# Kernel optimization log

Hardware: AMD Instinct MI355X
Metric: run time of the kernel (lower is better)

Reference implementation:

```python
import jax, jax.numpy as jnp
import numpy as np

EMBED_DIM = 1024
NUM_HEADS = 16
NUM_GROUPS = 4
HEAD_DIM = EMBED_DIM // NUM_HEADS
REPEAT = NUM_HEADS // NUM_GROUPS
MAX_TIME = 128
MAX_FREQ = 8


def build_relative_index(q_len, k_len, freq_size=MAX_FREQ, max_time=MAX_TIME, max_freq=MAX_FREQ):
    # static (numpy) construction; shapes are compile-time constants under jit
    q_time = q_len // max_freq
    k_time = k_len // max_freq
    qt = np.arange(q_time) + (k_time - q_time)
    q_coords = np.stack(np.meshgrid(qt, np.arange(freq_size), indexing='ij')).reshape(2, -1)
    k_coords = np.stack(np.meshgrid(np.arange(k_time), np.arange(freq_size), indexing='ij')).reshape(2, -1)
    rel = q_coords[:, :, None] - k_coords[:, None, :]  # [2, Nq, Nk]
    rel_t = np.clip(rel[0], -max_time + 1, max_time - 1) + max_time - 1
    rel_f = np.clip(rel[1], -max_freq + 1, max_freq - 1) + max_freq - 1
    return jnp.asarray(rel_t, jnp.int32), jnp.asarray(rel_f, jnp.int32)


def setup_inputs() -> dict:
    key = jax.random.key(0)
    ks = jax.random.split(key, 11)
    B, N, D, Nc = 2, 512, EMBED_DIM, 1536
    s = 0.02
    return {
        'q': jax.random.normal(ks[0], (B, N, D), jnp.float32),
        'k': jax.random.normal(ks[1], (B, N, D), jnp.float32),
        'v': jax.random.normal(ks[2], (B, N, D), jnp.float32),
        'attn_cache_k': jax.random.normal(ks[3], (B * NUM_HEADS, HEAD_DIM, Nc), jnp.float32),
        'attn_cache_v': jax.random.normal(ks[4], (B * NUM_HEADS, Nc, HEAD_DIM), jnp.float32),
        'Wq': jax.random.normal(ks[5], (D, D), jnp.float32) * s,
        'Wk': jax.random.normal(ks[6], (D, HEAD_DIM * NUM_GROUPS), jnp.float32) * s,
        'Wv': jax.random.normal(ks[7], (D, HEAD_DIM * NUM_GROUPS), jnp.float32) * s,
        'Wo': jax.random.normal(ks[8], (D, D), jnp.float32) * s,
        'emb_t': jax.random.normal(ks[9], (2 * MAX_TIME - 1, HEAD_DIM), jnp.float32) * s,
        'emb_f': jax.random.normal(ks[10], (2 * MAX_FREQ - 1, HEAD_DIM), jnp.float32) * s,
    }


def reference(q, k, v, attn_cache_k, attn_cache_v, Wq, Wk, Wv, Wo, emb_t, emb_f):
    B, N, D = q.shape
    H, G, hd, r = NUM_HEADS, NUM_GROUPS, HEAD_DIM, REPEAT
    # projections (no bias); head layout matches torch view: [B, N, H, hd] -> [B*H, N, hd]
    qp = (q @ Wq).reshape(B, N, H, hd).transpose(0, 2, 1, 3).reshape(B * H, N, hd)
    kp = (k @ Wk).reshape(B, N, G, hd).transpose(0, 2, 3, 1).reshape(B * G, hd, N)  # transposed K
    vp = (v @ Wv).reshape(B, N, G, hd).transpose(0, 2, 1, 3).reshape(B * G, N, hd)
    # GQA: repeat_interleave kv heads to query heads
    kp = jnp.repeat(kp, r, axis=0)
    vp = jnp.repeat(vp, r, axis=0)
    # streaming cache concat + slide
    k_full = jnp.concatenate([attn_cache_k, kp], axis=-1)            # [B*H, hd, Nk]
    new_cache_k = k_full[:, :, -attn_cache_k.shape[-1]:]
    v_full = jnp.concatenate([attn_cache_v, vp], axis=1)             # [B*H, Nk, hd]
    new_cache_v = v_full[:, -attn_cache_v.shape[1]:, :]
    Nk = k_full.shape[-1]
    qs = qp * (hd ** -0.5)
    scores = jnp.einsum('bid,bdj->bij', qs, k_full)                  # [B*H, N, Nk]
    rel_t, rel_f = build_relative_index(N, Nk)
    rel_emb = emb_t[rel_t] + emb_f[rel_f]                            # [N, Nk, hd]
    bias = jnp.einsum('bid,ijd->bij', qs, rel_emb)
    attn = jax.nn.softmax(scores + bias, axis=-1)
    ao = jnp.einsum('bij,bjd->bid', attn, v_full)                    # [B*H, N, hd]
    ao = ao.reshape(B, H, N, hd).transpose(2, 0, 1, 3).reshape(N, B, D)
    out = (ao @ Wo).transpose(1, 0, 2)                               # [B, N, D]
    return out, new_cache_k, new_cache_v
```

## Files before the change

### kernel.cpp

```cpp
#include <hip/hip_runtime.h>
#include <math.h>

typedef _Float16 half_t;
typedef _Float16 half8  __attribute__((ext_vector_type(8)));
typedef _Float16 half4v __attribute__((ext_vector_type(4)));
typedef float    floatx4 __attribute__((ext_vector_type(4)));

#define LOG2E 1.44269504088896f

static __device__ __forceinline__ floatx4 mfma16(half8 a, half8 b, floatx4 c) {
    return __builtin_amdgcn_mfma_f32_16x16x32_f16(a, b, c, 0, 0, 0);
}
static __device__ __forceinline__ floatx4 mfma16x16(half4v a, half4v b, floatx4 c) {
    return __builtin_amdgcn_mfma_f32_16x16x16f16(a, b, c, 0, 0, 0);
}

__global__ __launch_bounds__(256) void prep(const float* __restrict__ cache_k,
                                            const float* __restrict__ cache_v,
                                            const float* __restrict__ Wq,
                                            const float* __restrict__ Wk,
                                            const float* __restrict__ Wv,
                                            const float* __restrict__ Wo,
                                            const float* __restrict__ emb_t,
                                            const float* __restrict__ emb_f,
                                            half_t* __restrict__ Kc,
                                            half_t* __restrict__ Vc4,
                                            float* __restrict__ out_k,
                                            float* __restrict__ out_v,
                                            half_t* __restrict__ WqT,
                                            half_t* __restrict__ WkvT,
                                            half_t* __restrict__ WoT,
                                            half_t* __restrict__ embc)
{
    const int tid = threadIdx.x;
    const int z = blockIdx.z;
    __shared__ float t[64][65];
    if (z == 0) {
        const int bh = blockIdx.y, j0 = blockIdx.x * 64;
        const bool shift = (j0 >= 512);
        #pragma unroll
        for (int i2 = 0; i2 < 4; i2++) {
            int idx = i2 * 256 + tid;
            int d = idx >> 4, j4 = (idx & 15) * 4;
            float4 vv = *(const float4*)&cache_k[((size_t)bh * 64 + d) * 1536 + j0 + j4];
            *(float4*)&t[d][j4] = vv;
            if (shift) *(float4*)&out_k[((size_t)bh * 64 + d) * 1536 + j0 - 512 + j4] = vv;
        }
        __syncthreads();
        #pragma unroll
        for (int i2 = 0; i2 < 2; i2++) {
            int idx = i2 * 256 + tid;
            int j = idx >> 3, db = (idx & 7) * 8;
            half8 o;
            #pragma unroll
            for (int u = 0; u < 8; u++) o[u] = (half_t)t[db + u][j];
            *(half8*)&Kc[((size_t)bh * 1536 + j0 + j) * 64 + db] = o;
        }
    } else if (z == 1) {
        const int bh = blockIdx.y, j0 = blockIdx.x * 64;
        const bool shift = (j0 >= 512);
        #pragma unroll
        for (int i2 = 0; i2 < 4; i2++) {
            int idx = i2 * 256 + tid;
            int j = idx >> 4, d4 = (idx & 15) * 4;
            float4 vv = *(const float4*)&cache_v[((size_t)bh * 1536 + j0 + j) * 64 + d4];
            *(float4*)&t[j][d4] = vv;
            if (shift) *(float4*)&out_v[((size_t)bh * 1536 + j0 + j - 512) * 64 + d4] = vv;
        }
        __syncthreads();
        #pragma unroll
        for (int i2 = 0; i2 < 4; i2++) {
            int idx = i2 * 256 + tid;
            int jc = idx >> 6, d = idx & 63;
            half4v o;
            #pragma unroll
            for (int u = 0; u < 4; u++) o[u] = (half_t)t[jc * 4 + u][d];
            *(half4v*)&Vc4[(((size_t)bh * 384 + (j0 >> 2) + jc) * 64 + d) * 4] = o;
        }
    } else {
        const int id = blockIdx.y * 24 + blockIdx.x;
        const float* src; half_t* dst; int Ncols, n0, k0;
        if (id < 256)      { src = Wq; dst = WqT; Ncols = 1024; n0 = (id & 15) * 64; k0 = (id >> 4) * 64; }
        else if (id < 320) { int q2 = id - 256; src = Wk; dst = WkvT; Ncols = 256; n0 = (q2 & 3) * 64; k0 = (q2 >> 2) * 64; }
        else if (id < 384) { int q2 = id - 320; src = Wv; dst = WkvT + 256 * 1024; Ncols = 256; n0 = (q2 & 3) * 64; k0 = (q2 >> 2) * 64; }
        else if (id < 640) { int q2 = id - 384; src = Wo; dst = WoT; Ncols = 1024; n0 = (q2 & 15) * 64; k0 = (q2 >> 4) * 64; }
        else if (id < 720) {
            int idx = (id - 640) * 256 + tid;
            int row = idx >> 6, col = idx & 63;
            float val = 0.f;
            if (row < 255) val = emb_t[row * 64 + col];
            else if (row >= 256 && row < 271) val = emb_f[(row - 256) * 64 + col];
            embc[idx] = (half_t)val;
            return;
        } else return;
        #pragma unroll
        for (int i2 = 0; i2 < 4; i2++) {
            int idx = i2 * 256 + tid;
            int r = idx >> 4, c4 = (idx & 15) * 4;
            *(float4*)&t[r][c4] = *(const float4*)&src[(size_t)(k0 + r) * Ncols + n0 + c4];
        }
        __syncthreads();
        #pragma unroll
        for (int i2 = 0; i2 < 2; i2++) {
            int idx = i2 * 256 + tid;
            int n = idx >> 3, kb = (idx & 7) * 8;
            half8 o;
            #pragma unroll
            for (int u = 0; u < 8; u++) o[u] = (half_t)t[kb + u][n];
            *(half8*)&dst[(size_t)(n0 + n) * 1024 + k0 + kb] = o;
        }
    }
}

__global__ __launch_bounds__(512) void proj(int phase,
                                            const float* __restrict__ qin,
                                            const float* __restrict__ kin,
                                            const float* __restrict__ vin,
                                            const half_t* __restrict__ AO,
                                            const half_t* __restrict__ WqT,
                                            const half_t* __restrict__ WkvT,
                                            const half_t* __restrict__ WoT,
                                            half_t* __restrict__ qs_h,
                                            half_t* __restrict__ kp_h,
                                            half_t* __restrict__ Vp4,
                                            float* __restrict__ out,
                                            float* __restrict__ out_k,
                                            float* __restrict__ out_v)
{
    __shared__ __align__(16) half_t As[2][2][64 * 72];
    __shared__ __align__(16) half_t Bs[2][2][64 * 72];
    const int id = blockIdx.x;
    int task, m0, n0;
    const float* Af = nullptr; const half_t* Ah = nullptr; const half_t* Bt;
    if (phase == 1)      { task = 2; m0 = (id >> 4) * 64; n0 = (id & 15) * 64; Ah = AO; Bt = WoT; }
    else if (id < 256)   { task = 0; m0 = (id >> 4) * 64; n0 = (id & 15) * 64; Af = qin; Bt = WqT; }
    else { task = 1; int t = id - 256; m0 = (t >> 3) * 64; n0 = (t & 7) * 64;
           Af = (n0 < 256) ? kin : vin; Bt = WkvT; }

    const int tid = threadIdx.x;
    const int kh = tid >> 8, t8 = tid & 255;
    const int w4 = (tid >> 6) & 3, l = tid & 63;
    const int quad = l >> 4, lr = l & 15, wm = w4 >> 1, wn = w4 & 1;
    const int arow = t8 >> 2, acol = (t8 & 3) * 16;
    const int kbase = kh * 512;

    {
        int kk = kbase;
        if (Af) {
            float4 f0 = *(const float4*)&Af[(size_t)(m0 + arow) * 1024 + kk + acol];
            float4 f1 = *(const float4*)&Af[(size_t)(m0 + arow) * 1024 + kk + acol + 4];
            float4 f2 = *(const float4*)&Af[(size_t)(m0 + arow) * 1024 + kk + acol + 8];
            float4 f3 = *(const float4*)&Af[(size_t)(m0 + arow) * 1024 + kk + acol + 12];
            half8 h0, h1;
            h0[0]=(half_t)f0.x; h0[1]=(half_t)f0.y; h0[2]=(half_t)f0.z; h0[3]=(half_t)f0.w;
            h0[4]=(half_t)f1.x; h0[5]=(half_t)f1.y; h0[6]=(half_t)f1.z; h0[7]=(half_t)f1.w;
            h1[0]=(half_t)f2.x; h1[1]=(half_t)f2.y; h1[2]=(half_t)f2.z; h1[3]=(half_t)f2.w;
            h1[4]=(half_t)f3.x; h1[5]=(half_t)f3.y; h1[6]=(half_t)f3.z; h1[7]=(half_t)f3.w;
            *(half8*)&As[kh][0][arow * 72 + acol] = h0;
            *(half8*)&As[kh][0][arow * 72 + acol + 8] = h1;
        } else {
            *(half8*)&As[kh][0][arow * 72 + acol]     = *(const half8*)&Ah[(size_t)(m0 + arow) * 1024 + kk + acol];
            *(half8*)&As[kh][0][arow * 72 + acol + 8] = *(const half8*)&Ah[(size_t)(m0 + arow) * 1024 + kk + acol + 8];
        }
        *(half8*)&Bs[kh][0][arow * 72 + acol]     = *(const half8*)&Bt[(size_t)(n0 + arow) * 1024 + kk + acol];
        *(half8*)&Bs[kh][0][arow * 72 + acol + 8] = *(const half8*)&Bt[(size_t)(n0 + arow) * 1024 + kk + acol + 8];
    }
    __syncthreads();

    floatx4 zero = {0.f, 0.f, 0.f, 0.f};
    floatx4 acc[2][2];
    acc[0][0] = zero; acc[0][1] = zero; acc[1][0] = zero; acc[1][1] = zero;

    float4 pf0, pf1, pf2, pf3; half8 ph0, ph1, pb0, pb1;
    for (int it = 0; it < 8; ++it) {
        if (it < 7) {
            int kk = kbase + (it + 1) * 64;
            if (Af) {
                pf0 = *(const float4*)&Af[(size_t)(m0 + arow) * 1024 + kk + acol];
                pf1 = *(const float4*)&Af[(size_t)(m0 + arow) * 1024 + kk + acol + 4];
                pf2 = *(const float4*)&Af[(size_t)(m0 + arow) * 1024 + kk + acol + 8];
                pf3 = *(const float4*)&Af[(size_t)(m0 + arow) * 1024 + kk + acol + 12];
            } else {
                ph0 = *(const half8*)&Ah[(size_t)(m0 + arow) * 1024 + kk + acol];
                ph1 = *(const half8*)&Ah[(size_t)(m0 + arow) * 1024 + kk + acol + 8];
            }
            pb0 = *(const half8*)&Bt[(size_t)(n0 + arow) * 1024 + kk + acol];
            pb1 = *(const half8*)&Bt[(size_t)(n0 + arow) * 1024 + kk + acol + 8];
        }
        const half_t* Ab = &As[kh][it & 1][0];
        const half_t* Bb = &Bs[kh][it & 1][0];
        #pragma unroll
        for (int ks = 0; ks < 2; ++ks) {
            half8 a0 = *(const half8*)&Ab[(wm * 32 + lr) * 72 + ks * 32 + quad * 8];
            half8 a1 = *(const half8*)&Ab[(wm * 32 + 16 + lr) * 72 + ks * 32 + quad * 8];
            half8 b0 = *(const half8*)&Bb[(wn * 32 + lr) * 72 + ks * 32 + quad * 8];
            half8 b1 = *(const half8*)&Bb[(wn * 32 + 16 + lr) * 72 + ks * 32 + quad * 8];
            acc[0][0] = mfma16(a0, b0, acc[0][0]);
            acc[0][1] = mfma16(a0, b1, acc[0][1]);
            acc[1][0] = mfma16(a1, b0, acc[1][0]);
            acc[1][1] = mfma16(a1, b1, acc[1][1]);
        }
        __syncthreads();
        if (it < 7) {
            int buf = (it + 1) & 1;
            if (Af) {
                half8 h0, h1;
                h0[0]=(half_t)pf0.x; h0[1]=(half_t)pf0.y; h0[2]=(half_t)pf0.z; h0[3]=(half_t)pf0.w;
                h0[4]=(half_t)pf1.x; h0[5]=(half_t)pf1.y; h0[6]=(half_t)pf1.z; h0[7]=(half_t)pf1.w;
                h1[0]=(half_t)pf2.x; h1[1]=(half_t)pf2.y; h1[2]=(half_t)pf2.z; h1[3]=(half_t)pf2.w;
                h1[4]=(half_t)pf3.x; h1[5]=(half_t)pf3.y; h1[6]=(half_t)pf3.z; h1[7]=(half_t)pf3.w;
                *(half8*)&As[kh][buf][arow * 72 + acol] = h0;
                *(half8*)&As[kh][buf][arow * 72 + acol + 8] = h1;
            } else {
                *(half8*)&As[kh][buf][arow * 72 + acol] = ph0;
                *(half8*)&As[kh][buf][arow * 72 + acol + 8] = ph1;
            }
            *(half8*)&Bs[kh][buf][arow * 72 + acol] = pb0;
            *(half8*)&Bs[kh][buf][arow * 72 + acol + 8] = pb1;
            __syncthreads();
        }
    }

    float* M = (float*)&Bs[0][0][0];
    if (kh == 1) {
        #pragma unroll
        for (int mi = 0; mi < 2; mi++)
            #pragma unroll
            for (int ni = 0; ni < 2; ni++)
                #pragma unroll
                for (int r = 0; r < 4; r++)
                    M[(wm * 32 + mi * 16 + quad * 4 + r) * 66 + wn * 32 + ni * 16 + lr] = acc[mi][ni][r];
    }
    __syncthreads();
    if (kh == 0) {
        #pragma unroll
        for (int mi = 0; mi < 2; mi++)
            #pragma unroll
            for (int ni = 0; ni < 2; ni++)
                #pragma unroll
                for (int r = 0; r < 4; r++)
                    acc[mi][ni][r] += M[(wm * 32 + mi * 16 + quad * 4 + r) * 66 + wn * 32 + ni * 16 + lr];
    }

    if (task == 0) {
        if (kh == 0) {
            #pragma unroll
            for (int mi = 0; mi < 2; mi++)
                #pragma unroll
                for (int ni = 0; ni < 2; ni++)
                    #pragma unroll
                    for (int r = 0; r < 4; r++) {
                        int m = m0 + wm * 32 + mi * 16 + quad * 4 + r;
                        int n = n0 + wn * 32 + ni * 16 + lr;
                        qs_h[(size_t)m * 1024 + n] = (half_t)(acc[mi][ni][r] * (0.125f * LOG2E));
                    }
        }
    } else if (task == 2) {
        if (kh == 0) {
            #pragma unroll
            for (int mi = 0; mi < 2; mi++)
                #pragma unroll
                for (int ni = 0; ni < 2; ni++)
                    #pragma unroll
                    for (int r = 0; r < 4; r++) {
                        int m = m0 + wm * 32 + mi * 16 + quad * 4 + r;
                        int n = n0 + wn * 32 + ni * 16 + lr;
                        out[(size_t)m * 1024 + n] = acc[mi][ni][r];
                    }
        }
    } else {
        float* Ct = (float*)&As[0][0][0];
        if (kh == 0) {
            #pragma unroll
            for (int mi = 0; mi < 2; mi++)
                #pragma unroll
                for (int ni = 0; ni < 2; ni++)
                    #pragma unroll
                    for (int r = 0; r < 4; r++)
                        Ct[(wn * 32 + ni * 16 + lr) * 68 + wm * 32 + mi * 16 + quad * 4 + r] = acc[mi][ni][r];
        }
        __syncthreads();
        if (kh == 0) {
            const int b = m0 >> 9, jm0 = m0 & 511;
            if (n0 < 256) {
                int gg = n0 >> 6;
                {
                    int d = t8 >> 2, jc = (t8 & 3) * 16;
                    float4 vv[4];
                    #pragma unroll
                    for (int u = 0; u < 4; u++) vv[u] = *(float4*)&Ct[d * 68 + jc + u * 4];
                    #pragma unroll
                    for (int t = 0; t < 4; t++)
                        #pragma unroll
                        for (int u = 0; u < 4; u++)
                            *(float4*)&out_k[((size_t)((b * 16 + gg * 4 + t) * 64 + d)) * 1536 + 1024 + jm0 + jc + u * 4] = vv[u];
                }
                {
                    int j = t8 >> 2, dc = (t8 & 3) * 16;
                    half8 o0, o1;
                    #pragma unroll
                    for (int u = 0; u < 8; u++) o0[u] = (half_t)Ct[(dc + u) * 68 + j];
                    #pragma unroll
                    for (int u = 0; u < 8; u++) o1[u] = (half_t)Ct[(dc + 8 + u) * 68 + j];
                    *(half8*)&kp_h[((size_t)(b * 512 + jm0 + j)) * 256 + n0 + dc] = o0;
                    *(half8*)&kp_h[((size_t)(b * 512 + jm0 + j)) * 256 + n0 + dc + 8] = o1;
                }
            } else {
                int gg = (n0 - 256) >> 6;
                {
                    int j = t8 >> 2, dc = (t8 & 3) * 16;
                    float4 vv[4];
                    #pragma unroll
                    for (int u = 0; u < 4; u++) {
                        float4 x;
                        x.x = Ct[(dc + u * 4 + 0) * 68 + j];
                        x.y = Ct[(dc + u * 4 + 1) * 68 + j];
                        x.z = Ct[(dc + u * 4 + 2) * 68 + j];
                        x.w = Ct[(dc + u * 4 + 3) * 68 + j];
                        vv[u] = x;
                    }
                    #pragma unroll
                    for (int t = 0; t < 4; t++)
                        #pragma unroll
                        for (int u = 0; u < 4; u++)
                            *(float4*)&out_v[(((size_t)(b * 16 + gg * 4 + t) * 1536) + 1024 + jm0 + j) * 64 + dc + u * 4] = vv[u];
                }
                {
                    int d = t8 >> 2, jc16 = (t8 & 3) * 16;
                    #pragma unroll
                    for (int u = 0; u < 4; u++) {
                        half4v o;
                        #pragma unroll
                        for (int s2 = 0; s2 < 4; s2++) o[s2] = (half_t)Ct[d * 68 + jc16 + u * 4 + s2];
                        *(half4v*)&Vp4[(((size_t)(b * 4 + gg) * 128 + ((jm0 + jc16) >> 2) + u) * 64 + d) * 4] = o;
                    }
                }
            }
        }
    }
}

__global__ __launch_bounds__(512, 4) void flash(const half_t* __restrict__ qs_h,
                                                const half_t* __restrict__ Kc,
                                                const half_t* __restrict__ kp_h,
                                                const half_t* __restrict__ Vc4,
                                                const half_t* __restrict__ Vp4,
                                                const half_t* __restrict__ embc,
                                                half_t* __restrict__ AO)
{
    __shared__ __align__(16) unsigned char smem_raw[61824];
    half_t* bt = (half_t*)smem_raw;

    const int bh = blockIdx.x, b = bh >> 4, h = bh & 15, g = h >> 2;
    const int i0 = blockIdx.y * 32;
    const int tid = threadIdx.x, jh = tid >> 6, l = tid & 63;
    const int quad = l >> 4, lr = l & 15;

    half8 qf[2][2];
    #pragma unroll
    for (int ih = 0; ih < 2; ih++) {
        const half_t* qsrc = &qs_h[((size_t)(b * 512 + i0 + ih * 16 + lr)) * 1024 + h * 64];
        qf[ih][0] = *(const half8*)(qsrc + quad * 8);
        qf[ih][1] = *(const half8*)(qsrc + 32 + quad * 8);
    }

    floatx4 zero = {0.f, 0.f, 0.f, 0.f};
    {
        int ih = jh & 1;
        for (int tk = 4 + (jh >> 1); tk < 17; tk += 4) {
            floatx4 acc = zero;
            half8 e0 = *(const half8*)&embc[(size_t)(tk * 16 + lr) * 64 + quad * 8];
            half8 e1 = *(const half8*)&embc[(size_t)(tk * 16 + lr) * 64 + 32 + quad * 8];
            acc = mfma16(e0, qf[ih][0], acc);
            acc = mfma16(e1, qf[ih][1], acc);
            #pragma unroll
            for (int r = 0; r < 4; r++)
                bt[(ih * 16 + lr) * 210 + tk * 16 + quad * 4 + r - 64] = (half_t)acc[r];
        }
    }
    __syncthreads();

    float bfv[2][4];
    #pragma unroll
    for (int ih = 0; ih < 2; ih++)
        #pragma unroll
        for (int r = 0; r < 4; r++) {
            int f = (lr & 7) - ((quad & 1) * 4 + r) + 7;
            bfv[ih][r] = (float)bt[(ih * 16 + lr) * 210 + 192 + f];
        }
    const int qtr0 = (i0 + lr) >> 3;
    const int qtr1 = (i0 + 16 + lr) >> 3;

    floatx4 accO[2][4];
    #pragma unroll
    for (int ih = 0; ih < 2; ih++)
        #pragma unroll
        for (int ni = 0; ni < 4; ni++) accO[ih][ni] = zero;
    floatx4 accS[2];
    accS[0] = zero; accS[1] = zero;
    const half4v vone = {(half_t)1.f, (half_t)1.f, (half_t)1.f, (half_t)1.f};

    half8 kc0, kc1;
    {
        const half_t* kb = &Kc[((size_t)bh * 1536 + jh * 16 + lr) * 64];
        kc0 = *(const half8*)(kb + quad * 8);
        kc1 = *(const half8*)(kb + 32 + quad * 8);
    }

    for (int jt = 0; jt < 16; ++jt) {
        const int j0 = jt * 128;
        half4v vb[4];
        {
            const half_t* vbase; int jcb;
            if (j0 < 1536) { vbase = Vc4 + (size_t)bh * 98304;          jcb = j0 >> 2; }
            else           { vbase = Vp4 + (size_t)(b * 4 + g) * 32768; jcb = (j0 - 1536) >> 2; }
            const int jc = jcb + jh * 4 + quad;
            #pragma unroll
            for (int ni = 0; ni < 4; ni++)
                vb[ni] = *(const half4v*)&vbase[((size_t)jc * 64 + ni * 16 + lr) * 4];
        }
        half8 kn0, kn1;
        if (jt < 15) {
            const int j1 = j0 + 128;
            const half_t* kb = (j1 < 1536)
                ? &Kc[((size_t)bh * 1536 + j1 + jh * 16 + lr) * 64]
                : &kp_h[((size_t)(b * 512 + j1 - 1536 + jh * 16 + lr)) * 256 + g * 64];
            kn0 = *(const half8*)(kb + quad * 8);
            kn1 = *(const half8*)(kb + 32 + quad * 8);
        }

        floatx4 s[2];
        #pragma unroll
        for (int ih = 0; ih < 2; ih++) {
            s[ih] = mfma16(kc0, qf[ih][0], zero);
            s[ih] = mfma16(kc1, qf[ih][1], s[ih]);
        }
        const int ktb = jt * 16 + jh * 2 + (quad >> 1);
        #pragma unroll
        for (int ih = 0; ih < 2; ih++) {
            int toff = 255 + (ih ? qtr1 : qtr0) - ktb;
            toff = min(toff, 190);
            float tb = (float)bt[(ih * 16 + lr) * 210 + toff];
            #pragma unroll
            for (int r = 0; r < 4; r++)
                s[ih][r] = exp2f(s[ih][r] + tb + bfv[ih][r]);
        }
        #pragma unroll
        for (int ih = 0; ih < 2; ih++) {
            half4v pf;
            #pragma unroll
            for (int r = 0; r < 4; r++) pf[r] = (half_t)s[ih][r];
            accS[ih] = mfma16x16(pf, vone, accS[ih]);
            #pragma unroll
            for (int ni = 0; ni < 4; ni++)
                accO[ih][ni] = mfma16x16(pf, vb[ni], accO[ih][ni]);
        }
        if (jt < 15) { kc0 = kn0; kc1 = kn1; }
    }

    __syncthreads();
    float* Mf = (float*)smem_raw;
    float* Sf = Mf + 7 * 32 * 68;
    if (jh != 0) {
        const int p = jh - 1;
        #pragma unroll
        for (int ih = 0; ih < 2; ih++) {
            #pragma unroll
            for (int ni = 0; ni < 4; ni++)
                #pragma unroll
                for (int r = 0; r < 4; r++)
                    Mf[(p * 32 + ih * 16 + quad * 4 + r) * 68 + ni * 16 + lr] = accO[ih][ni][r];
            if (lr == 0) {
                #pragma unroll
                for (int r = 0; r < 4; r++)
                    Sf[p * 32 + ih * 16 + quad * 4 + r] = accS[ih][r];
            }
        }
    }
    __syncthreads();
    if (jh == 0) {
        #pragma unroll
        for (int ih = 0; ih < 2; ih++) {
            float inv[4];
            #pragma unroll
            for (int r = 0; r < 4; r++) {
                float t = accS[ih][r];
                #pragma unroll
                for (int p = 0; p < 7; p++) t += Sf[p * 32 + ih * 16 + quad * 4 + r];
                inv[r] = 1.0f / t;
            }
            #pragma unroll
            for (int ni = 0; ni < 4; ni++)
                #pragma unroll
                for (int r = 0; r < 4; r++) {
                    float o = accO[ih][ni][r];
                    #pragma unroll
                    for (int p = 0; p < 7; p++)
                        o += Mf[(p * 32 + ih * 16 + quad * 4 + r) * 68 + ni * 16 + lr];
                    int row = ih * 16 + quad * 4 + r;
                    AO[((size_t)(b * 512 + i0 + row)) * 1024 + h * 64 + ni * 16 + lr] =
                        (half_t)(o * inv[r]);
                }
        }
    }
}

extern "C" void kernel_launch(void* const* d_in, const int* in_sizes, int n_in,
                              void* d_out, int out_size, void* d_ws, size_t ws_size,
                              hipStream_t stream)
{
    const float* q       = (const float*)d_in[0];
    const float* k       = (const float*)d_in[1];
    const float* v       = (const float*)d_in[2];
    const float* cache_k = (const float*)d_in[3];
    const float* cache_v = (const float*)d_in[4];
    const float* Wq      = (const float*)d_in[5];
    const float* Wk      = (const float*)d_in[6];
    const float* Wv      = (const float*)d_in[7];
    const float* Wo      = (const float*)d_in[8];
    const float* emb_t   = (const float*)d_in[9];
    const float* emb_f   = (const float*)d_in[10];

    float* out   = (float*)d_out;
    float* out_k = out + 1048576;
    float* out_v = out_k + 3145728;

    half_t* ws = (half_t*)d_ws;
    half_t* qs_h = ws;
    half_t* kp_h = ws + 1048576;
    half_t* Vp4  = ws + 1310720;
    half_t* Kc   = ws + 1572864;
    half_t* Vc4  = ws + 4718592;
    half_t* WqT  = ws + 7864320;
    half_t* WkvT = ws + 8912896;
    half_t* WoT  = ws + 9437184;
    half_t* embc = ws + 10485760;
    half_t* AO   = ws + 10506240;

    prep<<<dim3(24, 32, 3), 256, 0, stream>>>(cache_k, cache_v, Wq, Wk, Wv, Wo,
                                              emb_t, emb_f, Kc, Vc4, out_k, out_v,
                                              WqT, WkvT, WoT, embc);
    proj<<<dim3(384), 512, 0, stream>>>(0, q, k, v, nullptr, WqT, WkvT, WoT,
                                        qs_h, kp_h, Vp4, out, out_k, out_v);
    flash<<<dim3(32, 16), 512, 0, stream>>>(qs_h, Kc, kp_h, Vc4, Vp4, embc, AO);
    proj<<<dim3(256), 512, 0, stream>>>(1, q, k, v, AO, WqT, WkvT, WoT,
                                        qs_h, kp_h, Vp4, out, out_k, out_v);
}
```

Measured before the change: 174.7 us.

## Overlap cache conversion with QKV projection and prefetch V one tile ahead

```diff
diff --git a/kernel.cpp b/kernel.cpp
--- a/kernel.cpp
+++ b/kernel.cpp
@@ -15,134 +15,74 @@
     return __builtin_amdgcn_mfma_f32_16x16x16f16(a, b, c, 0, 0, 0);
 }
 
-__global__ __launch_bounds__(256) void prep(const float* __restrict__ cache_k,
-                                            const float* __restrict__ cache_v,
-                                            const float* __restrict__ Wq,
-                                            const float* __restrict__ Wk,
-                                            const float* __restrict__ Wv,
-                                            const float* __restrict__ Wo,
-                                            const float* __restrict__ emb_t,
-                                            const float* __restrict__ emb_f,
-                                            half_t* __restrict__ Kc,
-                                            half_t* __restrict__ Vc4,
-                                            float* __restrict__ out_k,
-                                            float* __restrict__ out_v,
-                                            half_t* __restrict__ WqT,
-                                            half_t* __restrict__ WkvT,
-                                            half_t* __restrict__ WoT,
-                                            half_t* __restrict__ embc)
+__global__ __launch_bounds__(256) void prepw(const float* __restrict__ Wq,
+                                             const float* __restrict__ Wk,
+                                             const float* __restrict__ Wv,
+                                             const float* __restrict__ Wo,
+                                             const float* __restrict__ emb_t,
+                                             const float* __restrict__ emb_f,
+                                             half_t* __restrict__ WqT,
+                                             half_t* __restrict__ WkvT,
+                                             half_t* __restrict__ WoT,
+                                             half_t* __restrict__ embc)
 {
     const int tid = threadIdx.x;
-    const int z = blockIdx.z;
+    const int id = blockIdx.x;
     __shared__ float t[64][65];
-    if (z == 0) {
-        const int bh = blockIdx.y, j0 = blockIdx.x * 64;
-        const bool shift = (j0 >= 512);
-        #pragma unroll
-        for (int i2 = 0; i2 < 4; i2++) {
-            int idx = i2 * 256 + tid;
-            int d = idx >> 4, j4 = (idx & 15) * 4;
-            float4 vv = *(const float4*)&cache_k[((size_t)bh * 64 + d) * 1536 + j0 + j4];
-            *(float4*)&t[d][j4] = vv;
-            if (shift) *(float4*)&out_k[((size_t)bh * 64 + d) * 1536 + j0 - 512 + j4] = vv;
-        }
-        __syncthreads();
-        #pragma unroll
-        for (int i2 = 0; i2 < 2; i2++) {
-            int idx = i2 * 256 + tid;
-            int j = idx >> 3, db = (idx & 7) * 8;
-            half8 o;
-            #pragma unroll
-            for (int u = 0; u < 8; u++) o[u] = (half_t)t[db + u][j];
-            *(half8*)&Kc[((size_t)bh * 1536 + j0 + j) * 64 + db] = o;
-        }
-    } else if (z == 1) {
-        const int bh = blockIdx.y, j0 = blockIdx.x * 64;
-        const bool shift = (j0 >= 512);
-        #pragma unroll
-        for (int i2 = 0; i2 < 4; i2++) {
-            int idx = i2 * 256 + tid;
-            int j = idx >> 4, d4 = (idx & 15) * 4;
-            float4 vv = *(const float4*)&cache_v[((size_t)bh * 1536 + j0 + j) * 64 + d4];
-            *(float4*)&t[j][d4] = vv;
-            if (shift) *(float4*)&out_v[((size_t)bh * 1536 + j0 + j - 512) * 64 + d4] = vv;
-        }
-        __syncthreads();
-        #pragma unroll
-        for (int i2 = 0; i2 < 4; i2++) {
-            int idx = i2 * 256 + tid;
-            int jc = idx >> 6, d = idx & 63;
-            half4v o;
-            #pragma unroll
-            for (int u = 0; u < 4; u++) o[u] = (half_t)t[jc * 4 + u][d];
-            *(half4v*)&Vc4[(((size_t)bh * 384 + (j0 >> 2) + jc) * 64 + d) * 4] = o;
-        }
-    } else {
-        const int id = blockIdx.y * 24 + blockIdx.x;
-        const float* src; half_t* dst; int Ncols, n0, k0;
-        if (id < 256)      { src = Wq; dst = WqT; Ncols = 1024; n0 = (id & 15) * 64; k0 = (id >> 4) * 64; }
-        else if (id < 320) { int q2 = id - 256; src = Wk; dst = WkvT; Ncols = 256; n0 = (q2 & 3) * 64; k0 = (q2 >> 2) * 64; }
-        else if (id < 384) { int q2 = id - 320; src = Wv; dst = WkvT + 256 * 1024; Ncols = 256; n0 = (q2 & 3) * 64; k0 = (q2 >> 2) * 64; }
-        else if (id < 640) { int q2 = id - 384; src = Wo; dst = WoT; Ncols = 1024; n0 = (q2 & 15) * 64; k0 = (q2 >> 4) * 64; }
-        else if (id < 720) {
-            int idx = (id - 640) * 256 + tid;
-            int row = idx >> 6, col = idx & 63;
-            float val = 0.f;
-            if (row < 255) val = emb_t[row * 64 + col];
-            else if (row >= 256 && row < 271) val = emb_f[(row - 256) * 64 + col];
-            embc[idx] = (half_t)val;
-            return;
-        } else return;
-        #pragma unroll
-        for (int i2 = 0; i2 < 4; i2++) {
-            int idx = i2 * 256 + tid;
-            int r = idx >> 4, c4 = (idx & 15) * 4;
-            *(float4*)&t[r][c4] = *(const float4*)&src[(size_t)(k0 + r) * Ncols + n0 + c4];
-        }
-        __syncthreads();
-        #pragma unroll
-        for (int i2 = 0; i2 < 2; i2++) {
-            int idx = i2 * 256 + tid;
-            int n = idx >> 3, kb = (idx & 7) * 8;
-            half8 o;
-            #pragma unroll
-            for (int u = 0; u < 8; u++) o[u] = (half_t)t[kb + u][n];
-            *(half8*)&dst[(size_t)(n0 + n) * 1024 + k0 + kb] = o;
-        }
-    }
-}
-
-__global__ __launch_bounds__(512) void proj(int phase,
-                                            const float* __restrict__ qin,
-                                            const float* __restrict__ kin,
-                                            const float* __restrict__ vin,
-                                            const half_t* __restrict__ AO,
-                                            const half_t* __restrict__ WqT,
-                                            const half_t* __restrict__ WkvT,
-                                            const half_t* __restrict__ WoT,
-                                            half_t* __restrict__ qs_h,
-                                            half_t* __restrict__ kp_h,
-                                            half_t* __restrict__ Vp4,
-                                            float* __restrict__ out,
-                                            float* __restrict__ out_k,
-                                            float* __restrict__ out_v)
+    const float* src; half_t* dst; int Ncols, n0, k0;
+    if (id < 256)      { src = Wq; dst = WqT; Ncols = 1024; n0 = (id & 15) * 64; k0 = (id >> 4) * 64; }
+    else if (id < 320) { int q2 = id - 256; src = Wk; dst = WkvT; Ncols = 256; n0 = (q2 & 3) * 64; k0 = (q2 >> 2) * 64; }
+    else if (id < 384) { int q2 = id - 320; src = Wv; dst = WkvT + 256 * 1024; Ncols = 256; n0 = (q2 & 3) * 64; k0 = (q2 >> 2) * 64; }
+    else if (id < 640) { int q2 = id - 384; src = Wo; dst = WoT; Ncols = 1024; n0 = (q2 & 15) * 64; k0 = (q2 >> 4) * 64; }
+    else {
+        int idx = (id - 640) * 256 + tid;
+        int row = idx >> 6, col = idx & 63;
+        float val = 0.f;
+        if (row < 255) val = emb_t[row * 64 + col];
+        else if (row >= 256 && row < 271) val = emb_f[(row - 256) * 64 + col];
+        embc[idx] = (half_t)val;
+        return;
+    }
+    #pragma unroll
+    for (int i2 = 0; i2 < 4; i2++) {
+        int idx = i2 * 256 + tid;
+        int r = idx >> 4, c4 = (idx & 15) * 4;
+        *(float4*)&t[r][c4] = *(const float4*)&src[(size_t)(k0 + r) * Ncols + n0 + c4];
+    }
+    __syncthreads();
+    #pragma unroll
+    for (int i2 = 0; i2 < 2; i2++) {
+        int idx = i2 * 256 + tid;
+        int n = idx >> 3, kb = (idx & 7) * 8;
+        half8 o;
+        #pragma unroll
+        for (int u = 0; u < 8; u++) o[u] = (half_t)t[kb + u][n];
+        *(half8*)&dst[(size_t)(n0 + n) * 1024 + k0 + kb] = o;
+    }
+}
+
+static __device__ __forceinline__ void proj_core(int task, int m0, int n0,
+                                                 const float* __restrict__ Af,
+                                                 const half_t* __restrict__ Ah,
+                                                 const half_t* __restrict__ Bt,
+                                                 half_t* __restrict__ qs_h,
+                                                 half_t* __restrict__ kp_h,
+                                                 half_t* __restrict__ Vp4,
+                                                 float* __restrict__ out,
+                                                 float* __restrict__ out_k,
+                                                 float* __restrict__ out_v,
+                                                 half_t* sm, int tid)
 {
-    __shared__ __align__(16) half_t As[2][2][64 * 72];
-    __shared__ __align__(16) half_t Bs[2][2][64 * 72];
-    const int id = blockIdx.x;
-    int task, m0, n0;
-    const float* Af = nullptr; const half_t* Ah = nullptr; const half_t* Bt;
-    if (phase == 1)      { task = 2; m0 = (id >> 4) * 64; n0 = (id & 15) * 64; Ah = AO; Bt = WoT; }
-    else if (id < 256)   { task = 0; m0 = (id >> 4) * 64; n0 = (id & 15) * 64; Af = qin; Bt = WqT; }
-    else { task = 1; int t = id - 256; m0 = (t >> 3) * 64; n0 = (t & 7) * 64;
-           Af = (n0 < 256) ? kin : vin; Bt = WkvT; }
-
-    const int tid = threadIdx.x;
+    half_t* As = sm;
+    half_t* Bs = sm + 4 * 4608;
+
     const int kh = tid >> 8, t8 = tid & 255;
     const int w4 = (tid >> 6) & 3, l = tid & 63;
     const int quad = l >> 4, lr = l & 15, wm = w4 >> 1, wn = w4 & 1;
     const int arow = t8 >> 2, acol = (t8 & 3) * 16;
     const int kbase = kh * 512;
+    half_t* Ak = As + kh * 2 * 4608;
+    half_t* Bk = Bs + kh * 2 * 4608;
 
     {
         int kk = kbase;
@@ -156,14 +96,14 @@
             h0[4]=(half_t)f1.x; h0[5]=(half_t)f1.y; h0[6]=(half_t)f1.z; h0[7]=(half_t)f1.w;
             h1[0]=(half_t)f2.x; h1[1]=(half_t)f2.y; h1[2]=(half_t)f2.z; h1[3]=(half_t)f2.w;
             h1[4]=(half_t)f3.x; h1[5]=(half_t)f3.y; h1[6]=(half_t)f3.z; h1[7]=(half_t)f3.w;
-            *(half8*)&As[kh][0][arow * 72 + acol] = h0;
-            *(half8*)&As[kh][0][arow * 72 + acol + 8] = h1;
+            *(half8*)&Ak[arow * 72 + acol] = h0;
+            *(half8*)&Ak[arow * 72 + acol + 8] = h1;
         } else {
-            *(half8*)&As[kh][0][arow * 72 + acol]     = *(const half8*)&Ah[(size_t)(m0 + arow) * 1024 + kk + acol];
-            *(half8*)&As[kh][0][arow * 72 + acol + 8] = *(const half8*)&Ah[(size_t)(m0 + arow) * 1024 + kk + acol + 8];
-        }
-        *(half8*)&Bs[kh][0][arow * 72 + acol]     = *(const half8*)&Bt[(size_t)(n0 + arow) * 1024 + kk + acol];
-        *(half8*)&Bs[kh][0][arow * 72 + acol + 8] = *(const half8*)&Bt[(size_t)(n0 + arow) * 1024 + kk + acol + 8];
+            *(half8*)&Ak[arow * 72 + acol]     = *(const half8*)&Ah[(size_t)(m0 + arow) * 1024 + kk + acol];
+            *(half8*)&Ak[arow * 72 + acol + 8] = *(const half8*)&Ah[(size_t)(m0 + arow) * 1024 + kk + acol + 8];
+        }
+        *(half8*)&Bk[arow * 72 + acol]     = *(const half8*)&Bt[(size_t)(n0 + arow) * 1024 + kk + acol];
+        *(half8*)&Bk[arow * 72 + acol + 8] = *(const half8*)&Bt[(size_t)(n0 + arow) * 1024 + kk + acol + 8];
     }
     __syncthreads();
 
@@ -187,8 +127,8 @@
             pb0 = *(const half8*)&Bt[(size_t)(n0 + arow) * 1024 + kk + acol];
             pb1 = *(const half8*)&Bt[(size_t)(n0 + arow) * 1024 + kk + acol + 8];
         }
-        const half_t* Ab = &As[kh][it & 1][0];
-        const half_t* Bb = &Bs[kh][it & 1][0];
+        const half_t* Ab = Ak + (it & 1) * 4608;
+        const half_t* Bb = Bk + (it & 1) * 4608;
         #pragma unroll
         for (int ks = 0; ks < 2; ++ks) {
             half8 a0 = *(const half8*)&Ab[(wm * 32 + lr) * 72 + ks * 32 + quad * 8];
@@ -209,19 +149,19 @@
                 h0[4]=(half_t)pf1.x; h0[5]=(half_t)pf1.y; h0[6]=(half_t)pf1.z; h0[7]=(half_t)pf1.w;
                 h1[0]=(half_t)pf2.x; h1[1]=(half_t)pf2.y; h1[2]=(half_t)pf2.z; h1[3]=(half_t)pf2.w;
                 h1[4]=(half_t)pf3.x; h1[5]=(half_t)pf3.y; h1[6]=(half_t)pf3.z; h1[7]=(half_t)pf3.w;
-                *(half8*)&As[kh][buf][arow * 72 + acol] = h0;
-                *(half8*)&As[kh][buf][arow * 72 + acol + 8] = h1;
+                *(half8*)&Ak[buf * 4608 + arow * 72 + acol] = h0;
+                *(half8*)&Ak[buf * 4608 + arow * 72 + acol + 8] = h1;
             } else {
-                *(half8*)&As[kh][buf][arow * 72 + acol] = ph0;
-                *(half8*)&As[kh][buf][arow * 72 + acol + 8] = ph1;
+                *(half8*)&Ak[buf * 4608 + arow * 72 + acol] = ph0;
+                *(half8*)&Ak[buf * 4608 + arow * 72 + acol + 8] = ph1;
             }
-            *(half8*)&Bs[kh][buf][arow * 72 + acol] = pb0;
-            *(half8*)&Bs[kh][buf][arow * 72 + acol + 8] = pb1;
+            *(half8*)&Bk[buf * 4608 + arow * 72 + acol] = pb0;
+            *(half8*)&Bk[buf * 4608 + arow * 72 + acol + 8] = pb1;
             __syncthreads();
         }
     }
 
-    float* M = (float*)&Bs[0][0][0];
+    float* M = (float*)Bs;
     if (kh == 1) {
         #pragma unroll
         for (int mi = 0; mi < 2; mi++)
@@ -269,7 +209,7 @@
                     }
         }
     } else {
-        float* Ct = (float*)&As[0][0][0];
+        float* Ct = (float*)As;
         if (kh == 0) {
             #pragma unroll
             for (int mi = 0; mi < 2; mi++)
@@ -338,6 +278,97 @@
             }
         }
     }
+}
+
+__global__ __launch_bounds__(512) void stage1(const float* __restrict__ qin,
+                                              const float* __restrict__ kin,
+                                              const float* __restrict__ vin,
+                                              const float* __restrict__ cache_k,
+                                              const float* __restrict__ cache_v,
+                                              const half_t* __restrict__ WqT,
+                                              const half_t* __restrict__ WkvT,
+                                              half_t* __restrict__ qs_h,
+                                              half_t* __restrict__ kp_h,
+                                              half_t* __restrict__ Vp4,
+                                              half_t* __restrict__ Kc,
+                                              half_t* __restrict__ Vc4,
+                                              float* __restrict__ out_k,
+                                              float* __restrict__ out_v)
+{
+    __shared__ __align__(16) unsigned char sm[73728];
+    const int bid = blockIdx.x;
+    const int tid = threadIdx.x;
+
+    if (bid < 384) {
+        int task, m0, n0;
+        const float* Af; const half_t* Bt;
+        if (bid < 256) { task = 0; m0 = (bid >> 4) * 64; n0 = (bid & 15) * 64; Af = qin; Bt = WqT; }
+        else { task = 1; int t = bid - 256; m0 = (t >> 3) * 64; n0 = (t & 7) * 64;
+               Af = (n0 < 256) ? kin : vin; Bt = WkvT; }
+        proj_core(task, m0, n0, Af, nullptr, Bt, qs_h, kp_h, Vp4,
+                  nullptr, out_k, out_v, (half_t*)sm, tid);
+        return;
+    }
+
+    const int nb = bid - 384;
+    const int sub = tid >> 8, tl = tid & 255;
+    const int bx = nb % 24, by = nb / 24;
+    const int bh = by, j0 = bx * 64;
+    const bool shift = (j0 >= 512);
+    float (*t)[65] = (float(*)[65])(sm + sub * 16640);
+
+    if (sub == 0) {
+        #pragma unroll
+        for (int i2 = 0; i2 < 4; i2++) {
+            int idx = i2 * 256 + tl;
+            int d = idx >> 4, j4 = (idx & 15) * 4;
+            float4 vv = *(const float4*)&cache_k[((size_t)bh * 64 + d) * 1536 + j0 + j4];
+            *(float4*)&t[d][j4] = vv;
+            if (shift) *(float4*)&out_k[((size_t)bh * 64 + d) * 1536 + j0 - 512 + j4] = vv;
+        }
+    } else {
+        #pragma unroll
+        for (int i2 = 0; i2 < 4; i2++) {
+            int idx = i2 * 256 + tl;
+            int j = idx >> 4, d4 = (idx & 15) * 4;
+            float4 vv = *(const float4*)&cache_v[((size_t)bh * 1536 + j0 + j) * 64 + d4];
+            *(float4*)&t[j][d4] = vv;
+            if (shift) *(float4*)&out_v[((size_t)bh * 1536 + j0 + j - 512) * 64 + d4] = vv;
+        }
+    }
+    __syncthreads();
+    if (sub == 0) {
+        #pragma unroll
+        for (int i2 = 0; i2 < 2; i2++) {
+            int idx = i2 * 256 + tl;
+            int j = idx >> 3, db = (idx & 7) * 8;
+            half8 o;
+            #pragma unroll
+            for (int u = 0; u < 8; u++) o[u] = (half_t)t[db + u][j];
+            *(half8*)&Kc[((size_t)bh * 1536 + j0 + j) * 64 + db] = o;
+        }
+    } else {
+        #pragma unroll
+        for (int i2 = 0; i2 < 4; i2++) {
+            int idx = i2 * 256 + tl;
+            int jc = idx >> 6, d = idx & 63;
+            half4v o;
+            #pragma unroll
+            for (int u = 0; u < 4; u++) o[u] = (half_t)t[jc * 4 + u][d];
+            *(half4v*)&Vc4[(((size_t)bh * 384 + (j0 >> 2) + jc) * 64 + d) * 4] = o;
+        }
+    }
+}
+
+__global__ __launch_bounds__(512) void proj1(const half_t* __restrict__ AO,
+                                             const half_t* __restrict__ WoT,
+                                             float* __restrict__ out)
+{
+    __shared__ __align__(16) unsigned char sm[73728];
+    const int id = blockIdx.x;
+    const int m0 = (id >> 4) * 64, n0 = (id & 15) * 64;
+    proj_core(2, m0, n0, nullptr, AO, WoT, nullptr, nullptr, nullptr,
+              out, nullptr, nullptr, (half_t*)sm, threadIdx.x);
 }
 
 __global__ __launch_bounds__(512, 4) void flash(const half_t* __restrict__ qs_h,
@@ -400,33 +431,34 @@
     accS[0] = zero; accS[1] = zero;
     const half4v vone = {(half_t)1.f, (half_t)1.f, (half_t)1.f, (half_t)1.f};
 
-    half8 kc0, kc1;
+    half8 kc0, kc1; half4v vb[4];
     {
         const half_t* kb = &Kc[((size_t)bh * 1536 + jh * 16 + lr) * 64];
         kc0 = *(const half8*)(kb + quad * 8);
         kc1 = *(const half8*)(kb + 32 + quad * 8);
+        const half_t* vbase = Vc4 + (size_t)bh * 98304;
+        const int jc = jh * 4 + quad;
+        #pragma unroll
+        for (int ni = 0; ni < 4; ni++)
+            vb[ni] = *(const half4v*)&vbase[((size_t)jc * 64 + ni * 16 + lr) * 4];
     }
 
     for (int jt = 0; jt < 16; ++jt) {
-        const int j0 = jt * 128;
-        half4v vb[4];
-        {
-            const half_t* vbase; int jcb;
-            if (j0 < 1536) { vbase = Vc4 + (size_t)bh * 98304;          jcb = j0 >> 2; }
-            else           { vbase = Vp4 + (size_t)(b * 4 + g) * 32768; jcb = (j0 - 1536) >> 2; }
-            const int jc = jcb + jh * 4 + quad;
-            #pragma unroll
-            for (int ni = 0; ni < 4; ni++)
-                vb[ni] = *(const half4v*)&vbase[((size_t)jc * 64 + ni * 16 + lr) * 4];
-        }
-        half8 kn0, kn1;
+        half8 kn0, kn1; half4v vn[4];
         if (jt < 15) {
-            const int j1 = j0 + 128;
+            const int j1 = (jt + 1) * 128;
             const half_t* kb = (j1 < 1536)
                 ? &Kc[((size_t)bh * 1536 + j1 + jh * 16 + lr) * 64]
                 : &kp_h[((size_t)(b * 512 + j1 - 1536 + jh * 16 + lr)) * 256 + g * 64];
             kn0 = *(const half8*)(kb + quad * 8);
             kn1 = *(const half8*)(kb + 32 + quad * 8);
+            const half_t* vbase; int jcb;
+            if (j1 < 1536) { vbase = Vc4 + (size_t)bh * 98304;          jcb = j1 >> 2; }
+            else           { vbase = Vp4 + (size_t)(b * 4 + g) * 32768; jcb = (j1 - 1536) >> 2; }
+            const int jc = jcb + jh * 4 + quad;
+            #pragma unroll
+            for (int ni = 0; ni < 4; ni++)
+                vn[ni] = *(const half4v*)&vbase[((size_t)jc * 64 + ni * 16 + lr) * 4];
         }
 
         floatx4 s[2];
@@ -455,7 +487,11 @@
             for (int ni = 0; ni < 4; ni++)
                 accO[ih][ni] = mfma16x16(pf, vb[ni], accO[ih][ni]);
         }
-        if (jt < 15) { kc0 = kn0; kc1 = kn1; }
+        if (jt < 15) {
+            kc0 = kn0; kc1 = kn1;
+            #pragma unroll
+            for (int ni = 0; ni < 4; ni++) vb[ni] = vn[ni];
+        }
     }
 
     __syncthreads();
@@ -537,12 +573,11 @@
     half_t* embc = ws + 10485760;
     half_t* AO   = ws + 10506240;
 
-    prep<<<dim3(24, 32, 3), 256, 0, stream>>>(cache_k, cache_v, Wq, Wk, Wv, Wo,
-                                              emb_t, emb_f, Kc, Vc4, out_k, out_v,
-                                              WqT, WkvT, WoT, embc);
-    proj<<<dim3(384), 512, 0, stream>>>(0, q, k, v, nullptr, WqT, WkvT, WoT,
-                                        qs_h, kp_h, Vp4, out, out_k, out_v);
+    prepw<<<dim3(720), 256, 0, stream>>>(Wq, Wk, Wv, Wo, emb_t, emb_f,
+                                         WqT, WkvT, WoT, embc);
+    stage1<<<dim3(1152), 512, 0, stream>>>(q, k, v, cache_k, cache_v,
+                                           WqT, WkvT, qs_h, kp_h, Vp4,
+                                           Kc, Vc4, out_k, out_v);
     flash<<<dim3(32, 16), 512, 0, stream>>>(qs_h, Kc, kp_h, Vc4, Vp4, embc, AO);
-    proj<<<dim3(256), 512, 0, stream>>>(1, q, k, v, AO, WqT, WkvT, WoT,
-                                        qs_h, kp_h, Vp4, out, out_k, out_v);
-}
+    proj1<<<dim3(256), 512, 0, stream>>>(AO, WoT, out);
+}
```

Result: faster. 169.1 us (-3.3%).
